# Kernel tuning notes

Hardware: AMD Instinct MI355X
Metric: run time of the kernel (lower is better)

## Reference

```python
import jax, jax.numpy as jnp
import numpy as np

MAX_USERS = 100000
T = 2            # edge_type_count
D = 100          # edge_dim
B = 512
IN_DIM = 200
OUT_DIM = 200
PARTS = [[3, 15], [3, 15, 105, 945]]   # per-schema neighbor partition sizes
RAND_PARTS = [3, 15]
TOTAL_P = sum(PARTS[0]) + sum(PARTS[1])


def _layernorm(x, g, b, eps=1e-6):
    mu = x.mean(axis=-1, keepdims=True)
    var = ((x - mu) ** 2).mean(axis=-1, keepdims=True)
    return (x - mu) / jnp.sqrt(var + eps) * g + b


def _mha(x, Wq, Wk, Wv, Wf, g, b):
    # single-head attention over the second-to-last axis (n_head=1, d_k=d_v=D).
    # NOTE: original only layer-norms q (k, v use the raw input); residual add at end.
    residual = x
    q = _layernorm(x, g, b) @ Wq
    k = x @ Wk
    v = x @ Wv
    attn = jax.nn.softmax(jnp.einsum('...qd,...kd->...qk', q / jnp.sqrt(D), k), axis=-1)
    out = jnp.einsum('...qk,...kd->...qd', attn, v) @ Wf
    return out + residual, attn


def _mean_agg(Ws, Wn, self_x, neigh_x):
    # GraphSAGE-style mean aggregator: relu(concat(self @ Ws, mean(neigh) @ Wn)).
    # neigh_x has shape [N*r, D]; reshape to [N, r, D] and mean over the fanout r.
    n, d = self_x.shape
    neigh_mean = neigh_x.reshape(n, -1, d).mean(axis=1)
    return jax.nn.relu(jnp.concatenate([self_x @ Ws, neigh_mean @ Wn], axis=-1))


def _schema_view(idx, parts, Wself, Wneigh, type_embed, nodeids, neigh_s):
    # neigh_s: [B, T, sum(parts)] node ids for meta-path idx. Returns [B, T, D].
    # Faithful to type_embed[neigh][:, :, :, :, idx, :][:, t, :, t, :] but gathers
    # only the needed (type t, schema idx) slice instead of the huge dense tensor.
    chunks = jnp.split(neigh_s, np.cumsum(parts)[:-1].tolist(), axis=2)
    specs = []
    for t in range(T):
        feats = [type_embed[nodeids, t, idx]]                    # [B, D]
        for c in chunks:
            feats.append(type_embed[c[:, t, :], t, idx].reshape(-1, D))
        for l in range(len(parts)):
            feats = [_mean_agg(Wself[l], Wneigh[l], feats[k], feats[k + 1])
                     for k in range(len(feats) - 1)]
        specs.append(feats[0])
    return jnp.stack(specs, axis=1)


def setup_inputs() -> dict:
    ks = jax.random.split(jax.random.key(0), 32)
    unif = lambda i, s: jax.random.uniform(ks[i], s, dtype=jnp.float32, minval=-1.0, maxval=1.0)
    nrm = lambda i, s, sc=0.1: jax.random.normal(ks[i], s, dtype=jnp.float32) * sc
    inp = {}
    inp['nodeids'] = jax.random.randint(ks[0], (B,), 0, MAX_USERS)
    inp['edgetype'] = jnp.stack([jnp.arange(B), jax.random.randint(ks[1], (B,), 0, T)])
    inp['neighbors'] = jax.random.randint(ks[2], (B, T, TOTAL_P), 0, MAX_USERS)
    inp['random_neighbors'] = jax.random.randint(ks[3], (B, sum(RAND_PARTS)), 0, MAX_USERS)
    inp['base_embed'] = unif(4, (MAX_USERS, IN_DIM))
    inp['type_embed'] = unif(5, (MAX_USERS, T, len(PARTS), D))
    inp['rw_embed'] = unif(6, (MAX_USERS, D))
    inp['reflect'] = nrm(7, (T, D, OUT_DIM), 1.0 / float(np.sqrt(IN_DIM)))
    inp['agg0_self'] = nrm(8, (2, D, D // 2)); inp['agg0_neigh'] = nrm(9, (2, D, D // 2))
    inp['agg1_self'] = nrm(10, (4, D, D // 2)); inp['agg1_neigh'] = nrm(11, (4, D, D // 2))
    inp['rand_self'] = nrm(12, (2, D, D // 2)); inp['rand_neigh'] = nrm(13, (2, D, D // 2))
    inp['vWq'] = nrm(14, (D, D)); inp['vWk'] = nrm(15, (D, D)); inp['vWv'] = nrm(16, (D, D)); inp['vWf'] = nrm(17, (D, D))
    inp['vg'] = jnp.ones((D,), jnp.float32); inp['vb'] = jnp.zeros((D,), jnp.float32)
    inp['mWq'] = nrm(18, (D, D)); inp['mWk'] = nrm(19, (D, D)); inp['mWv'] = nrm(20, (D, D)); inp['mWf'] = nrm(21, (D, D))
    inp['mg'] = jnp.ones((D,), jnp.float32); inp['mb'] = jnp.zeros((D,), jnp.float32)
    return inp


def reference(nodeids, edgetype, neighbors, random_neighbors, base_embed, type_embed,
              rw_embed, reflect, agg0_self, agg0_neigh, agg1_self, agg1_neigh,
              rand_self, rand_neigh, vWq, vWk, vWv, vWf, vg, vb,
              mWq, mWk, mWv, mWf, mg, mb):
    # per-metapath views [B, T, D]
    spec0 = _schema_view(0, PARTS[0], agg0_self, agg0_neigh, type_embed, nodeids,
                         neighbors[:, :, :sum(PARTS[0])])
    spec1 = _schema_view(1, PARTS[1], agg1_self, agg1_neigh, type_embed, nodeids,
                         neighbors[:, :, sum(PARTS[0]):])
    # random-walk view [B, D]
    feats = [rw_embed[nodeids]]
    for c in jnp.split(random_neighbors, np.cumsum(RAND_PARTS)[:-1].tolist(), axis=1):
        feats.append(rw_embed[c].reshape(-1, D))
    for l in range(len(RAND_PARTS)):
        feats = [_mean_agg(rand_self[l], rand_neigh[l], feats[k], feats[k + 1])
                 for k in range(len(feats) - 1)]
    rview = feats[0]
    mv = jnp.stack([spec0, spec1], axis=1)                                   # [B, 2, T, D]
    mv = jnp.concatenate([mv, jnp.broadcast_to(rview[:, None, None, :], (B, 1, T, D))], axis=1)  # [B, 3, T, D]
    mv, _ = _mha(mv, vWq, vWk, vWv, vWf, vg, vb)                             # view attn over type axis T
    mt, _ = _mha(jnp.swapaxes(mv, 1, 2), mWq, mWk, mWv, mWf, mg, mb)         # meta attn over view axis
    pooled = jnp.swapaxes(mt, 1, 2).mean(axis=1)                             # [B, T, D]
    sel = pooled[edgetype[0], edgetype[1]]                                   # [B, D]
    out = jnp.einsum('bd,bdo->bo', sel, reflect[edgetype[1]])                # [B, OUT_DIM]
    res = base_embed[nodeids] + out
    return res / jnp.maximum(jnp.linalg.norm(res, axis=1, keepdims=True), 1e-12)
```

## Files before the change

### kernel.cpp

```cpp
#include <hip/hip_runtime.h>
#include <math.h>


#define NBATCH 512
#define TOTALP 1086
#define RPB 32
#define XSTR 204
#define WSTR 112

struct Seg {
  const float* emb;
  const float* selfp;
  const float* neighp;
  const int*   ids_s;
  const int*   ids_n;
  const float* Ws;
  const float* Wn;
  float*       outp;
  int ss, so;
  int ns, no;
  int estride;
  int ostride;
  int c;
  int r;
  int blk_begin;
};

struct KArgs { Seg seg[14]; int n; };

__global__ __launch_bounds__(256) void agg_kernel(KArgs P) {
  __shared__ float Wsh[100 * WSTR];
  __shared__ float xsh[RPB * XSTR];
  __shared__ int   ids_s_sh[RPB];
  __shared__ int   ids_n_sh[RPB * 9];

  const int blk = blockIdx.x, tid = threadIdx.x;
  int si = 0;
  for (int i = 1; i < P.n; ++i)
    if (blk >= P.seg[i].blk_begin) si = i;
  const Seg sg = P.seg[si];
  const int j0 = (blk - sg.blk_begin) * RPB;
  const int c = sg.c, r = sg.r;

  for (int u = tid; u < 5000; u += 256) {
    int e = u / 50, cc = u - e * 50;
    Wsh[e * WSTR + cc]      = sg.Ws[u];
    Wsh[e * WSTR + 56 + cc] = sg.Wn[u];
  }
  for (int u = tid; u < 1200; u += 256) {
    int e = u / 12, p = u - e * 12;
    Wsh[e * WSTR + (p < 6 ? 50 + p : 100 + p)] = 0.f;
  }
  if (sg.emb) {
    if (tid < RPB) {
      int j = j0 + tid, b = j / c, pos = j - b * c;
      ids_s_sh[tid] = sg.ids_s[(long)b * sg.ss + sg.so + pos];
    }
    for (int u = tid; u < RPB * r; u += 256) {
      int row = u / r, q = u - row * r;
      int j = j0 + row, b = j / c, pos = j - b * c;
      ids_n_sh[u] = sg.ids_n[(long)b * sg.ns + sg.no + pos * r + q];
    }
  }
  __syncthreads();

  const float rinv = 1.f / (float)r;
  for (int u = tid; u < RPB * 25; u += 256) {
    int row = u / 25, q4 = (u - row * 25) * 4;
    float sx, sy, sz, sw, mx = 0.f, my = 0.f, mz = 0.f, mw = 0.f;
    if (sg.emb) {
      const float4 s4 = *(const float4*)(sg.emb + (long)ids_s_sh[row] * sg.estride + q4);
      sx = s4.x; sy = s4.y; sz = s4.z; sw = s4.w;
      for (int rr = 0; rr < r; ++rr) {
        const float4 t = *(const float4*)(sg.emb + (long)ids_n_sh[row * r + rr] * sg.estride + q4);
        mx += t.x; my += t.y; mz += t.z; mw += t.w;
      }
    } else {
      long j = j0 + row;
      const float4 s4 = *(const float4*)(sg.selfp + j * 100 + q4);
      sx = s4.x; sy = s4.y; sz = s4.z; sw = s4.w;
      for (int rr = 0; rr < r; ++rr) {
        const float4 t = *(const float4*)(sg.neighp + (j * r + rr) * 100 + q4);
        mx += t.x; my += t.y; mz += t.z; mw += t.w;
      }
    }
    float4 sv; sv.x = sx; sv.y = sy; sv.z = sz; sv.w = sw;
    float4 mv; mv.x = mx * rinv; mv.y = my * rinv; mv.z = mz * rinv; mv.w = mw * rinv;
    *(float4*)&xsh[row * XSTR + q4]       = sv;
    *(float4*)&xsh[row * XSTR + 100 + q4] = mv;
  }
  __syncthreads();

  if (tid < 224) {
    const int rg = tid / 28, cq = tid - rg * 28;
    const int wcol = 4 * cq;
    const int xoff = (cq < 14) ? 0 : 100;
    float acc[4][4];
#pragma unroll
    for (int i = 0; i < 4; ++i) { acc[i][0] = acc[i][1] = acc[i][2] = acc[i][3] = 0.f; }
    const float* xb = &xsh[(rg * 4) * XSTR + xoff];
#pragma unroll 4
    for (int e = 0; e < 100; ++e) {
      const float4 wv = *(const float4*)&Wsh[e * WSTR + wcol];
#pragma unroll
      for (int i = 0; i < 4; ++i) {
        const float a = xb[i * XSTR + e];
        acc[i][0] = fmaf(a, wv.x, acc[i][0]);
        acc[i][1] = fmaf(a, wv.y, acc[i][1]);
        acc[i][2] = fmaf(a, wv.z, acc[i][2]);
        acc[i][3] = fmaf(a, wv.w, acc[i][3]);
      }
    }
    const int cl = (cq < 14) ? cq : cq - 14;
    if (cl < 13) {
      const int cbase = (cq < 14 ? 0 : 50) + 4 * cl;
      for (int i = 0; i < 4; ++i) {
        const long j = j0 + rg * 4 + i;
        float* op = sg.outp + j * (long)sg.ostride + cbase;
        if (cl < 12) {
          float4 o;
          o.x = fmaxf(acc[i][0], 0.f); o.y = fmaxf(acc[i][1], 0.f);
          o.z = fmaxf(acc[i][2], 0.f); o.w = fmaxf(acc[i][3], 0.f);
          *(float4*)op = o;
        } else {
          op[0] = fmaxf(acc[i][0], 0.f);
          op[1] = fmaxf(acc[i][1], 0.f);
        }
      }
    }
  }
}

__device__ __forceinline__ void attn_step(
    float* xs, int base, int rs, int n,
    const float* Wq, const float* Wk, const float* Wv, const float* Wf,
    const float* g, const float* bb,
    float* ln, float* qq, float* kk, float* vv, float* ot,
    float* sc, float* musd, float* wsh, int tid)
{
  if (tid < n) {
    float mu = 0.f;
    for (int d = 0; d < 100; ++d) mu += xs[base + tid * rs + d];
    mu *= 0.01f;
    float var = 0.f;
    for (int d = 0; d < 100; ++d) {
      float t = xs[base + tid * rs + d] - mu; var = fmaf(t, t, var);
    }
    var *= 0.01f;
    musd[tid * 2]     = mu;
    musd[tid * 2 + 1] = rsqrtf(var + 1e-6f);
  }
  __syncthreads();
  for (int o = tid; o < n * 100; o += 128) {
    int i = o / 100, d = o - i * 100;
    ln[o] = (xs[base + i * rs + d] - musd[i * 2]) * musd[i * 2 + 1] * g[d] + bb[d];
  }
  __syncthreads();

  const bool act = tid < n * 25;
  const int  i   = tid / 25;
  const int  d4  = 4 * (tid - i * 25);
  float aq[4] = {0,0,0,0}, ak[4] = {0,0,0,0}, av[4] = {0,0,0,0};
  for (int ch = 0; ch < 2; ++ch) {
    for (int u = tid; u < 1250; u += 128) {
      int el = u / 25, dd = 4 * (u - el * 25);
      *(float4*)&wsh[el * 300 + dd]       = *(const float4*)&Wq[(ch * 50 + el) * 100 + dd];
      *(float4*)&wsh[el * 300 + 100 + dd] = *(const float4*)&Wk[(ch * 50 + el) * 100 + dd];
      *(float4*)&wsh[el * 300 + 200 + dd] = *(const float4*)&Wv[(ch * 50 + el) * 100 + dd];
    }
    __syncthreads();
    if (act) {
      for (int el = 0; el < 50; ++el) {
        const float lnv = ln[i * 100 + ch * 50 + el];
        const float xv  = xs[base + i * rs + ch * 50 + el];
        const float4 wq = *(const float4*)&wsh[el * 300 + d4];
        const float4 wk = *(const float4*)&wsh[el * 300 + 100 + d4];
        const float4 wv = *(const float4*)&wsh[el * 300 + 200 + d4];
        aq[0] = fmaf(lnv, wq.x, aq[0]); aq[1] = fmaf(lnv, wq.y, aq[1]);
        aq[2] = fmaf(lnv, wq.z, aq[2]); aq[3] = fmaf(lnv, wq.w, aq[3]);
        ak[0] = fmaf(xv,  wk.x, ak[0]); ak[1] = fmaf(xv,  wk.y, ak[1]);
        ak[2] = fmaf(xv,  wk.z, ak[2]); ak[3] = fmaf(xv,  wk.w, ak[3]);
        av[0] = fmaf(xv,  wv.x, av[0]); av[1] = fmaf(xv,  wv.y, av[1]);
        av[2] = fmaf(xv,  wv.z, av[2]); av[3] = fmaf(xv,  wv.w, av[3]);
      }
    }
    __syncthreads();
  }
  if (act) {
#pragma unroll
    for (int jj = 0; jj < 4; ++jj) {
      qq[i * 100 + d4 + jj] = aq[jj];
      kk[i * 100 + d4 + jj] = ak[jj];
      vv[i * 100 + d4 + jj] = av[jj];
    }
  }
  __syncthreads();

  if (tid < n * n) {
    int qi = tid / n, u = tid - qi * n;
    float s = 0.f;
    for (int d = 0; d < 100; ++d) s = fmaf(qq[qi * 100 + d], kk[u * 100 + d], s);
    sc[tid] = s * 0.1f;
  }
  __syncthreads();
  if (tid < n) {
    float mx = sc[tid * n];
    for (int u = 1; u < n; ++u) mx = fmaxf(mx, sc[tid * n + u]);
    float sm = 0.f;
    for (int u = 0; u < n; ++u) {
      float e = expf(sc[tid * n + u] - mx); sc[tid * n + u] = e; sm += e;
    }
    float inv = 1.f / sm;
    for (int u = 0; u < n; ++u) sc[tid * n + u] *= inv;
  }
  __syncthreads();
  for (int o = tid; o < n * 100; o += 128) {
    int ii = o / 100, d = o - ii * 100;
    float a = 0.f;
    for (int u = 0; u < n; ++u) a = fmaf(sc[ii * n + u], vv[u * 100 + d], a);
    ot[o] = a;
  }
  __syncthreads();

  float af[4] = {0,0,0,0};
  for (int ch = 0; ch < 2; ++ch) {
    for (int u = tid; u < 1250; u += 128) {
      int el = u / 25, dd = 4 * (u - el * 25);
      *(float4*)&wsh[el * 100 + dd] = *(const float4*)&Wf[(ch * 50 + el) * 100 + dd];
    }
    __syncthreads();
    if (act) {
      for (int el = 0; el < 50; ++el) {
        const float ov = ot[i * 100 + ch * 50 + el];
        const float4 wf = *(const float4*)&wsh[el * 100 + d4];
        af[0] = fmaf(ov, wf.x, af[0]); af[1] = fmaf(ov, wf.y, af[1]);
        af[2] = fmaf(ov, wf.z, af[2]); af[3] = fmaf(ov, wf.w, af[3]);
      }
    }
    __syncthreads();
  }
  if (act) {
#pragma unroll
    for (int jj = 0; jj < 4; ++jj)
      xs[base + i * rs + d4 + jj] += af[jj];
  }
  __syncthreads();
}

__global__ __launch_bounds__(128) void attn_final_kernel(
    const float* __restrict__ spec, const float* __restrict__ rview,
    const int* __restrict__ nodeids, const int* __restrict__ edgetype,
    const float* __restrict__ base_embed, const float* __restrict__ reflect,
    const float* vWq, const float* vWk, const float* vWv, const float* vWf,
    const float* vg, const float* vb,
    const float* mWq, const float* mWk, const float* mWv, const float* mWf,
    const float* mg, const float* mb,
    float* __restrict__ out)
{
  __shared__ float xs[600], ln[300], qq[300], kk[300], vv[300], ot[300];
  __shared__ float sc[9], musd[6], r200[200], pooled[200], nrmv[1];
  __shared__ float wsh[15000];
  const int b = blockIdx.x, tid = threadIdx.x;

  for (int o = tid; o < 600; o += 128) {
    int v = o / 200, rem = o - v * 200;
    xs[o] = (v < 2) ? spec[(long)b * 400 + o] : rview[(long)b * 100 + (rem % 100)];
  }
  __syncthreads();

  for (int v = 0; v < 3; ++v)
    attn_step(xs, v * 200, 100, 2, vWq, vWk, vWv, vWf, vg, vb,
              ln, qq, kk, vv, ot, sc, musd, wsh, tid);
  for (int t = 0; t < 2; ++t)
    attn_step(xs, t * 100, 200, 3, mWq, mWk, mWv, mWf, mg, mb,
              ln, qq, kk, vv, ot, sc, musd, wsh, tid);

  for (int o = tid; o < 200; o += 128)
    pooled[o] = (xs[o] + xs[200 + o] + xs[400 + o]) * (1.f / 3.f);
  __syncthreads();

  const int  et  = edgetype[NBATCH + b];
  const long nid = nodeids[b];

  float ar[4] = {0,0,0,0};
  if (tid < 50) {
    const float4 be = *(const float4*)&base_embed[nid * 200 + 4 * tid];
    ar[0] = be.x; ar[1] = be.y; ar[2] = be.z; ar[3] = be.w;
  }
  for (int ch = 0; ch < 2; ++ch) {
    for (int u = tid; u < 2500; u += 128) {
      int dl = u / 50, oo = 4 * (u - dl * 50);
      *(float4*)&wsh[dl * 200 + oo] =
          *(const float4*)&reflect[((long)et * 100 + ch * 50 + dl) * 200 + oo];
    }
    __syncthreads();
    if (tid < 50) {
      for (int dl = 0; dl < 50; ++dl) {
        const float pv = pooled[et * 100 + ch * 50 + dl];
        const float4 rv = *(const float4*)&wsh[dl * 200 + 4 * tid];
        ar[0] = fmaf(pv, rv.x, ar[0]); ar[1] = fmaf(pv, rv.y, ar[1]);
        ar[2] = fmaf(pv, rv.z, ar[2]); ar[3] = fmaf(pv, rv.w, ar[3]);
      }
    }
    __syncthreads();
  }
  if (tid < 50) {
    r200[4 * tid]     = ar[0]; r200[4 * tid + 1] = ar[1];
    r200[4 * tid + 2] = ar[2]; r200[4 * tid + 3] = ar[3];
  }
  __syncthreads();
  if (tid == 0) {
    float ss = 0.f;
    for (int o = 0; o < 200; ++o) ss = fmaf(r200[o], r200[o], ss);
    nrmv[0] = 1.f / fmaxf(sqrtf(ss), 1e-12f);
  }
  __syncthreads();
  for (int o = tid; o < 200; o += 128)
    out[(long)b * 200 + o] = r200[o] * nrmv[0];
}

extern "C" void kernel_launch(void* const* d_in, const int* in_sizes, int n_in,
                              void* d_out, int out_size, void* d_ws, size_t ws_size,
                              hipStream_t stream) {
  (void)in_sizes; (void)n_in; (void)out_size; (void)ws_size;
  const int*   nodeids          = (const int*)d_in[0];
  const int*   edgetype         = (const int*)d_in[1];
  const int*   neighbors        = (const int*)d_in[2];
  const int*   random_neighbors = (const int*)d_in[3];
  const float* base_embed       = (const float*)d_in[4];
  const float* type_embed       = (const float*)d_in[5];
  const float* rw_embed         = (const float*)d_in[6];
  const float* reflect          = (const float*)d_in[7];
  const float* agg0_self        = (const float*)d_in[8];
  const float* agg0_neigh       = (const float*)d_in[9];
  const float* agg1_self        = (const float*)d_in[10];
  const float* agg1_neigh       = (const float*)d_in[11];
  const float* rand_self        = (const float*)d_in[12];
  const float* rand_neigh       = (const float*)d_in[13];
  const float* vWq = (const float*)d_in[14];
  const float* vWk = (const float*)d_in[15];
  const float* vWv = (const float*)d_in[16];
  const float* vWf = (const float*)d_in[17];
  const float* vg  = (const float*)d_in[18];
  const float* vb  = (const float*)d_in[19];
  const float* mWq = (const float*)d_in[20];
  const float* mWk = (const float*)d_in[21];
  const float* mWv = (const float*)d_in[22];
  const float* mWf = (const float*)d_in[23];
  const float* mg  = (const float*)d_in[24];
  const float* mb  = (const float*)d_in[25];

  float* ws = (float*)d_ws;
  const long S1r = 147L * NBATCH;
  auto rp = [&](long rows) { return ws + rows * 100; };
  float* spec_f  = ws + 306L * NBATCH * 100;
  float* rview_f = spec_f + (long)NBATCH * 400;

  const int  OFF1[4] = {18, 21, 36, 141};
  const int  FAN1[4] = {3, 5, 7, 9};
  const int  C1[4]   = {1, 3, 15, 105};
  const long CUM1[4]  = {0, 1, 4, 19};
  const long CUM1b[3] = {0, 1, 4};

  KArgs A; long acc = 0;
  auto addg = [&](const float* emb, int estride,
                  const int* isrc, int ss, int so, int c,
                  const int* insrc, int nstr, int no, int r,
                  const float* Ws, const float* Wn, float* outp, int ostride) {
    Seg& s = A.seg[A.n++];
    s.emb = emb; s.selfp = nullptr; s.neighp = nullptr;
    s.ids_s = isrc; s.ids_n = insrc;
    s.Ws = Ws; s.Wn = Wn; s.outp = outp;
    s.ss = ss; s.so = so; s.ns = nstr; s.no = no;
    s.estride = estride; s.ostride = ostride;
    s.c = c; s.r = r; s.blk_begin = (int)acc;
    acc += (long)c * NBATCH / RPB;
  };
  auto addd = [&](const float* selfp, const float* neighp, int c, int r,
                  const float* Ws, const float* Wn, float* outp, int ostride) {
    Seg& s = A.seg[A.n++];
    s.emb = nullptr; s.selfp = selfp; s.neighp = neighp;
    s.ids_s = nullptr; s.ids_n = nullptr;
    s.Ws = Ws; s.Wn = Wn; s.outp = outp;
    s.ss = 0; s.so = 0; s.ns = 0; s.no = 0; s.estride = 0; s.ostride = ostride;
    s.c = c; s.r = r; s.blk_begin = (int)acc;
    acc += (long)c * NBATCH / RPB;
  };

  A.n = 0; acc = 0;
  for (int t = 0; t < 2; ++t)
    for (int k = 0; k < 4; ++k) {
      const float* emb = type_embed + (t * 2 + 1) * 100;
      if (k == 0)
        addg(emb, 400, nodeids, 1, 0, 1,
             neighbors, 2 * TOTALP, t * TOTALP + OFF1[k], FAN1[k],
             agg1_self, agg1_neigh, rp(t * S1r + CUM1[k] * NBATCH), 100);
      else
        addg(emb, 400, neighbors, 2 * TOTALP, t * TOTALP + OFF1[k - 1], C1[k],
             neighbors, 2 * TOTALP, t * TOTALP + OFF1[k], FAN1[k],
             agg1_self, agg1_neigh, rp(t * S1r + CUM1[k] * NBATCH), 100);
    }
  for (int t = 0; t < 2; ++t)
    for (int k = 0; k < 2; ++k) {
      const float* emb = type_embed + (t * 2 + 0) * 100;
      long obase = 294L * NBATCH + (long)t * 4 * NBATCH + (k == 0 ? 0 : 1) * NBATCH;
      if (k == 0)
        addg(emb, 400, nodeids, 1, 0, 1,
             neighbors, 2 * TOTALP, t * TOTALP + 0, 3,
             agg0_self, agg0_neigh, rp(obase), 100);
      else
        addg(emb, 400, neighbors, 2 * TOTALP, t * TOTALP + 0, 3,
             neighbors, 2 * TOTALP, t * TOTALP + 3, 5,
             agg0_self, agg0_neigh, rp(obase), 100);
    }
  for (int k = 0; k < 2; ++k) {
    long obase = 302L * NBATCH + (k == 0 ? 0 : 1) * NBATCH;
    if (k == 0)
      addg(rw_embed, 100, nodeids, 1, 0, 1,
           random_neighbors, 18, 0, 3, rand_self, rand_neigh, rp(obase), 100);
    else
      addg(rw_embed, 100, random_neighbors, 18, 0, 3,
           random_neighbors, 18, 3, 5, rand_self, rand_neigh, rp(obase), 100);
  }
  agg_kernel<<<dim3((unsigned)acc), dim3(256), 0, stream>>>(A);

  A.n = 0; acc = 0;
  for (int t = 0; t < 2; ++t)
    for (int k = 0; k < 3; ++k)
      addd(rp(t * S1r + CUM1[k] * NBATCH), rp(t * S1r + CUM1[k + 1] * NBATCH),
           C1[k], FAN1[k], agg1_self + 5000, agg1_neigh + 5000,
           rp(t * S1r + 124L * NBATCH + CUM1b[k] * NBATCH), 100);
  for (int t = 0; t < 2; ++t)
    addd(rp(294L * NBATCH + (long)t * 4 * NBATCH),
         rp(294L * NBATCH + (long)t * 4 * NBATCH + NBATCH),
         1, 3, agg0_self + 5000, agg0_neigh + 5000, spec_f + t * 100, 400);
  addd(rp(302L * NBATCH), rp(303L * NBATCH), 1, 3,
       rand_self + 5000, rand_neigh + 5000, rview_f, 100);
  agg_kernel<<<dim3((unsigned)acc), dim3(256), 0, stream>>>(A);

  A.n = 0; acc = 0;
  for (int t = 0; t < 2; ++t)
    for (int k = 0; k < 2; ++k)
      addd(rp(t * S1r + 124L * NBATCH + CUM1b[k] * NBATCH),
           rp(t * S1r + 124L * NBATCH + CUM1b[k + 1] * NBATCH),
           C1[k], FAN1[k], agg1_self + 10000, agg1_neigh + 10000,
           rp(t * S1r + 143L * NBATCH + (k == 0 ? 0 : 1) * NBATCH), 100);
  agg_kernel<<<dim3((unsigned)acc), dim3(256), 0, stream>>>(A);

  A.n = 0; acc = 0;
  for (int t = 0; t < 2; ++t)
    addd(rp(t * S1r + 143L * NBATCH), rp(t * S1r + 144L * NBATCH),
         1, 3, agg1_self + 15000, agg1_neigh + 15000,
         spec_f + 200 + t * 100, 400);
  agg_kernel<<<dim3((unsigned)acc), dim3(256), 0, stream>>>(A);

  attn_final_kernel<<<dim3(NBATCH), dim3(128), 0, stream>>>(
      spec_f, rview_f, nodeids, edgetype, base_embed, reflect,
      vWq, vWk, vWv, vWf, vg, vb, mWq, mWk, mWv, mWf, mg, mb,
      (float*)d_out);
}
```

Measured before the change: 657.5 us.

## Compute only the selected edge-type path and read weights directly from global memory

The attention kernel now carries only the query row for the selected edge type through view attention, and only the selected type slice through meta attention. Rows that never reach the output are skipped. It moves to 256 threads with wave-shuffle reductions and drops the large shared-memory weight staging in favour of direct global (L2-cached) weight reads. The aggregation kernel likewise drops its shared-memory weight staging and the padding writes, reading Ws/Wn straight from global memory, which lowers LDS use and may raise occupancy. The trade-off is more global/L2 traffic for weight reads.

New measurement: 707.6 us. 7.6% more time.

```diff
diff --git a/kernel.cpp b/kernel.cpp
--- a/kernel.cpp
+++ b/kernel.cpp
@@ -6,7 +6,6 @@
 #define TOTALP 1086
 #define RPB 32
 #define XSTR 204
-#define WSTR 112
 
 struct Seg {
   const float* emb;
@@ -29,7 +28,6 @@
 struct KArgs { Seg seg[14]; int n; };
 
 __global__ __launch_bounds__(256) void agg_kernel(KArgs P) {
-  __shared__ float Wsh[100 * WSTR];
   __shared__ float xsh[RPB * XSTR];
   __shared__ int   ids_s_sh[RPB];
   __shared__ int   ids_n_sh[RPB * 9];
@@ -42,15 +40,6 @@
   const int j0 = (blk - sg.blk_begin) * RPB;
   const int c = sg.c, r = sg.r;
 
-  for (int u = tid; u < 5000; u += 256) {
-    int e = u / 50, cc = u - e * 50;
-    Wsh[e * WSTR + cc]      = sg.Ws[u];
-    Wsh[e * WSTR + 56 + cc] = sg.Wn[u];
-  }
-  for (int u = tid; u < 1200; u += 256) {
-    int e = u / 12, p = u - e * 12;
-    Wsh[e * WSTR + (p < 6 ? 50 + p : 100 + p)] = 0.f;
-  }
   if (sg.emb) {
     if (tid < RPB) {
       int j = j0 + tid, b = j / c, pos = j - b * c;
@@ -61,8 +50,8 @@
       int j = j0 + row, b = j / c, pos = j - b * c;
       ids_n_sh[u] = sg.ids_n[(long)b * sg.ns + sg.no + pos * r + q];
     }
-  }
-  __syncthreads();
+    __syncthreads();
+  }
 
   const float rinv = 1.f / (float)r;
   for (int u = tid; u < RPB * 25; u += 256) {
@@ -91,232 +80,211 @@
   }
   __syncthreads();
 
-  if (tid < 224) {
-    const int rg = tid / 28, cq = tid - rg * 28;
-    const int wcol = 4 * cq;
-    const int xoff = (cq < 14) ? 0 : 100;
+  if (tid < 208) {
+    const int rg = tid / 26, hq = tid - rg * 26;
+    const int half = hq / 13, q = hq - half * 13;
+    const int col = 4 * q;
+    const float* W = half ? sg.Wn : sg.Ws;
+    const float* xb = &xsh[(rg * 4) * XSTR + half * 100];
     float acc[4][4];
 #pragma unroll
     for (int i = 0; i < 4; ++i) { acc[i][0] = acc[i][1] = acc[i][2] = acc[i][3] = 0.f; }
-    const float* xb = &xsh[(rg * 4) * XSTR + xoff];
-#pragma unroll 4
-    for (int e = 0; e < 100; ++e) {
-      const float4 wv = *(const float4*)&Wsh[e * WSTR + wcol];
+    if (q < 12) {
+#pragma unroll 2
+      for (int e = 0; e < 100; ++e) {
+        const float4 wv = *(const float4*)&W[e * 50 + col];
 #pragma unroll
-      for (int i = 0; i < 4; ++i) {
-        const float a = xb[i * XSTR + e];
-        acc[i][0] = fmaf(a, wv.x, acc[i][0]);
-        acc[i][1] = fmaf(a, wv.y, acc[i][1]);
-        acc[i][2] = fmaf(a, wv.z, acc[i][2]);
-        acc[i][3] = fmaf(a, wv.w, acc[i][3]);
-      }
-    }
-    const int cl = (cq < 14) ? cq : cq - 14;
-    if (cl < 13) {
-      const int cbase = (cq < 14 ? 0 : 50) + 4 * cl;
-      for (int i = 0; i < 4; ++i) {
-        const long j = j0 + rg * 4 + i;
-        float* op = sg.outp + j * (long)sg.ostride + cbase;
-        if (cl < 12) {
-          float4 o;
-          o.x = fmaxf(acc[i][0], 0.f); o.y = fmaxf(acc[i][1], 0.f);
-          o.z = fmaxf(acc[i][2], 0.f); o.w = fmaxf(acc[i][3], 0.f);
-          *(float4*)op = o;
-        } else {
-          op[0] = fmaxf(acc[i][0], 0.f);
-          op[1] = fmaxf(acc[i][1], 0.f);
+        for (int i = 0; i < 4; ++i) {
+          const float a = xb[i * XSTR + e];
+          acc[i][0] = fmaf(a, wv.x, acc[i][0]);
+          acc[i][1] = fmaf(a, wv.y, acc[i][1]);
+          acc[i][2] = fmaf(a, wv.z, acc[i][2]);
+          acc[i][3] = fmaf(a, wv.w, acc[i][3]);
         }
       }
+    } else {
+#pragma unroll 2
+      for (int e = 0; e < 100; ++e) {
+        const float2 wv = *(const float2*)&W[e * 50 + 48];
+#pragma unroll
+        for (int i = 0; i < 4; ++i) {
+          const float a = xb[i * XSTR + e];
+          acc[i][0] = fmaf(a, wv.x, acc[i][0]);
+          acc[i][1] = fmaf(a, wv.y, acc[i][1]);
+        }
+      }
+    }
+    const int ocol = half * 50 + col;
+    for (int i = 0; i < 4; ++i) {
+      const long j = j0 + rg * 4 + i;
+      float* op = sg.outp + j * (long)sg.ostride + ocol;
+      if (q < 12) {
+        float4 o;
+        o.x = fmaxf(acc[i][0], 0.f); o.y = fmaxf(acc[i][1], 0.f);
+        o.z = fmaxf(acc[i][2], 0.f); o.w = fmaxf(acc[i][3], 0.f);
+        *(float4*)op = o;
+      } else {
+        float2 o;
+        o.x = fmaxf(acc[i][0], 0.f); o.y = fmaxf(acc[i][1], 0.f);
+        *(float2*)op = o;
+      }
     }
   }
 }
 
-__device__ __forceinline__ void attn_step(
-    float* xs, int base, int rs, int n,
-    const float* Wq, const float* Wk, const float* Wv, const float* Wf,
-    const float* g, const float* bb,
-    float* ln, float* qq, float* kk, float* vv, float* ot,
-    float* sc, float* musd, float* wsh, int tid)
-{
-  if (tid < n) {
-    float mu = 0.f;
-    for (int d = 0; d < 100; ++d) mu += xs[base + tid * rs + d];
-    mu *= 0.01f;
-    float var = 0.f;
-    for (int d = 0; d < 100; ++d) {
-      float t = xs[base + tid * rs + d] - mu; var = fmaf(t, t, var);
-    }
-    var *= 0.01f;
-    musd[tid * 2]     = mu;
-    musd[tid * 2 + 1] = rsqrtf(var + 1e-6f);
-  }
-  __syncthreads();
-  for (int o = tid; o < n * 100; o += 128) {
-    int i = o / 100, d = o - i * 100;
-    ln[o] = (xs[base + i * rs + d] - musd[i * 2]) * musd[i * 2 + 1] * g[d] + bb[d];
-  }
-  __syncthreads();
-
-  const bool act = tid < n * 25;
-  const int  i   = tid / 25;
-  const int  d4  = 4 * (tid - i * 25);
-  float aq[4] = {0,0,0,0}, ak[4] = {0,0,0,0}, av[4] = {0,0,0,0};
-  for (int ch = 0; ch < 2; ++ch) {
-    for (int u = tid; u < 1250; u += 128) {
-      int el = u / 25, dd = 4 * (u - el * 25);
-      *(float4*)&wsh[el * 300 + dd]       = *(const float4*)&Wq[(ch * 50 + el) * 100 + dd];
-      *(float4*)&wsh[el * 300 + 100 + dd] = *(const float4*)&Wk[(ch * 50 + el) * 100 + dd];
-      *(float4*)&wsh[el * 300 + 200 + dd] = *(const float4*)&Wv[(ch * 50 + el) * 100 + dd];
-    }
-    __syncthreads();
-    if (act) {
-      for (int el = 0; el < 50; ++el) {
-        const float lnv = ln[i * 100 + ch * 50 + el];
-        const float xv  = xs[base + i * rs + ch * 50 + el];
-        const float4 wq = *(const float4*)&wsh[el * 300 + d4];
-        const float4 wk = *(const float4*)&wsh[el * 300 + 100 + d4];
-        const float4 wv = *(const float4*)&wsh[el * 300 + 200 + d4];
-        aq[0] = fmaf(lnv, wq.x, aq[0]); aq[1] = fmaf(lnv, wq.y, aq[1]);
-        aq[2] = fmaf(lnv, wq.z, aq[2]); aq[3] = fmaf(lnv, wq.w, aq[3]);
-        ak[0] = fmaf(xv,  wk.x, ak[0]); ak[1] = fmaf(xv,  wk.y, ak[1]);
-        ak[2] = fmaf(xv,  wk.z, ak[2]); ak[3] = fmaf(xv,  wk.w, ak[3]);
-        av[0] = fmaf(xv,  wv.x, av[0]); av[1] = fmaf(xv,  wv.y, av[1]);
-        av[2] = fmaf(xv,  wv.z, av[2]); av[3] = fmaf(xv,  wv.w, av[3]);
-      }
-    }
-    __syncthreads();
-  }
-  if (act) {
+__device__ __forceinline__ float wave_sum_bcast(float p) {
 #pragma unroll
-    for (int jj = 0; jj < 4; ++jj) {
-      qq[i * 100 + d4 + jj] = aq[jj];
-      kk[i * 100 + d4 + jj] = ak[jj];
-      vv[i * 100 + d4 + jj] = av[jj];
-    }
-  }
-  __syncthreads();
-
-  if (tid < n * n) {
-    int qi = tid / n, u = tid - qi * n;
-    float s = 0.f;
-    for (int d = 0; d < 100; ++d) s = fmaf(qq[qi * 100 + d], kk[u * 100 + d], s);
-    sc[tid] = s * 0.1f;
-  }
-  __syncthreads();
-  if (tid < n) {
-    float mx = sc[tid * n];
-    for (int u = 1; u < n; ++u) mx = fmaxf(mx, sc[tid * n + u]);
-    float sm = 0.f;
-    for (int u = 0; u < n; ++u) {
-      float e = expf(sc[tid * n + u] - mx); sc[tid * n + u] = e; sm += e;
-    }
-    float inv = 1.f / sm;
-    for (int u = 0; u < n; ++u) sc[tid * n + u] *= inv;
-  }
-  __syncthreads();
-  for (int o = tid; o < n * 100; o += 128) {
-    int ii = o / 100, d = o - ii * 100;
-    float a = 0.f;
-    for (int u = 0; u < n; ++u) a = fmaf(sc[ii * n + u], vv[u * 100 + d], a);
-    ot[o] = a;
-  }
-  __syncthreads();
-
-  float af[4] = {0,0,0,0};
-  for (int ch = 0; ch < 2; ++ch) {
-    for (int u = tid; u < 1250; u += 128) {
-      int el = u / 25, dd = 4 * (u - el * 25);
-      *(float4*)&wsh[el * 100 + dd] = *(const float4*)&Wf[(ch * 50 + el) * 100 + dd];
-    }
-    __syncthreads();
-    if (act) {
-      for (int el = 0; el < 50; ++el) {
-        const float ov = ot[i * 100 + ch * 50 + el];
-        const float4 wf = *(const float4*)&wsh[el * 100 + d4];
-        af[0] = fmaf(ov, wf.x, af[0]); af[1] = fmaf(ov, wf.y, af[1]);
-        af[2] = fmaf(ov, wf.z, af[2]); af[3] = fmaf(ov, wf.w, af[3]);
-      }
-    }
-    __syncthreads();
-  }
-  if (act) {
-#pragma unroll
-    for (int jj = 0; jj < 4; ++jj)
-      xs[base + i * rs + d4 + jj] += af[jj];
-  }
-  __syncthreads();
+  for (int off = 32; off; off >>= 1) p += __shfl_down(p, off);
+  return __shfl(p, 0);
 }
 
-__global__ __launch_bounds__(128) void attn_final_kernel(
+__global__ __launch_bounds__(256) void attn_final_kernel(
     const float* __restrict__ spec, const float* __restrict__ rview,
     const int* __restrict__ nodeids, const int* __restrict__ edgetype,
     const float* __restrict__ base_embed, const float* __restrict__ reflect,
-    const float* vWq, const float* vWk, const float* vWv, const float* vWf,
-    const float* vg, const float* vb,
-    const float* mWq, const float* mWk, const float* mWv, const float* mWf,
-    const float* mg, const float* mb,
+    const float* __restrict__ vWq, const float* __restrict__ vWk,
+    const float* __restrict__ vWv, const float* __restrict__ vWf,
+    const float* __restrict__ vg, const float* __restrict__ vb,
+    const float* __restrict__ mWq, const float* __restrict__ mWk,
+    const float* __restrict__ mWv, const float* __restrict__ mWf,
+    const float* __restrict__ mg, const float* __restrict__ mb,
     float* __restrict__ out)
 {
-  __shared__ float xs[600], ln[300], qq[300], kk[300], vv[300], ot[300];
-  __shared__ float sc[9], musd[6], r200[200], pooled[200], nrmv[1];
-  __shared__ float wsh[15000];
+  __shared__ float xs[600], lnb[300], qq[300], kk[300], vv[300], ot[300];
+  __shared__ float sc[9], musd[6], pooled[100], r200[200], nrmv[1];
   const int b = blockIdx.x, tid = threadIdx.x;
-
-  for (int o = tid; o < 600; o += 128) {
+  const int et = edgetype[NBATCH + b];
+  const int nid = nodeids[b];
+
+  for (int o = tid; o < 600; o += 256) {
     int v = o / 200, rem = o - v * 200;
     xs[o] = (v < 2) ? spec[(long)b * 400 + o] : rview[(long)b * 100 + (rem % 100)];
   }
   __syncthreads();
 
-  for (int v = 0; v < 3; ++v)
-    attn_step(xs, v * 200, 100, 2, vWq, vWk, vWv, vWf, vg, vb,
-              ln, qq, kk, vv, ot, sc, musd, wsh, tid);
-  for (int t = 0; t < 2; ++t)
-    attn_step(xs, t * 100, 200, 3, mWq, mWk, mWv, mWf, mg, mb,
-              ln, qq, kk, vv, ot, sc, musd, wsh, tid);
-
-  for (int o = tid; o < 200; o += 128)
-    pooled[o] = (xs[o] + xs[200 + o] + xs[400 + o]) * (1.f / 3.f);
+  for (int v = 0; v < 3; ++v) {
+    float* xq = xs + v * 200 + et * 100;
+    if (tid < 64) {
+      float p = (tid < 50) ? xq[tid] + xq[tid + 50] : 0.f;
+      p = wave_sum_bcast(p);
+      float mu = p * 0.01f, vr = 0.f;
+      if (tid < 50) { float a = xq[tid] - mu, c2 = xq[tid + 50] - mu; vr = a * a + c2 * c2; }
+      vr = wave_sum_bcast(vr);
+      if (tid == 0) { musd[0] = mu; musd[1] = rsqrtf(vr * 0.01f + 1e-6f); }
+    }
+    __syncthreads();
+    if (tid < 100) lnb[tid] = (xq[tid] - musd[0]) * musd[1] * vg[tid] + vb[tid];
+    __syncthreads();
+    for (int o = tid; o < 500; o += 256) {
+      const int m = o / 100, d = o - m * 100;
+      const float* xr; const float* W; float* dst;
+      if (m == 0)      { xr = lnb;                          W = vWq; dst = qq; }
+      else if (m <= 2) { xr = xs + v * 200 + (m - 1) * 100; W = vWk; dst = kk + (m - 1) * 100; }
+      else             { xr = xs + v * 200 + (m - 3) * 100; W = vWv; dst = vv + (m - 3) * 100; }
+      float a = 0.f;
+      for (int e = 0; e < 100; ++e) a = fmaf(xr[e], W[e * 100 + d], a);
+      dst[d] = a;
+    }
+    __syncthreads();
+    if (tid < 2) {
+      float s = 0.f;
+      for (int d = 0; d < 100; ++d) s = fmaf(qq[d], kk[tid * 100 + d], s);
+      sc[tid] = s * 0.1f;
+    }
+    __syncthreads();
+    if (tid == 0) {
+      float mx = fmaxf(sc[0], sc[1]);
+      float e0 = __expf(sc[0] - mx), e1 = __expf(sc[1] - mx);
+      float inv = 1.f / (e0 + e1);
+      sc[0] = e0 * inv; sc[1] = e1 * inv;
+    }
+    __syncthreads();
+    if (tid < 100) ot[tid] = sc[0] * vv[tid] + sc[1] * vv[100 + tid];
+    __syncthreads();
+    if (tid < 100) {
+      float a = 0.f;
+      for (int e = 0; e < 100; ++e) a = fmaf(ot[e], vWf[e * 100 + tid], a);
+      xq[tid] += a;
+    }
+    __syncthreads();
+  }
+
+  {
+    const int w = tid >> 6, l = tid & 63;
+    if (w < 3) {
+      const float* xr = xs + w * 200 + et * 100;
+      float p = (l < 50) ? xr[l] + xr[l + 50] : 0.f;
+      p = wave_sum_bcast(p);
+      float mu = p * 0.01f, vr = 0.f;
+      if (l < 50) { float a = xr[l] - mu, c2 = xr[l + 50] - mu; vr = a * a + c2 * c2; }
+      vr = wave_sum_bcast(vr);
+      if (l == 0) { musd[w * 2] = mu; musd[w * 2 + 1] = rsqrtf(vr * 0.01f + 1e-6f); }
+    }
+    __syncthreads();
+    for (int o = tid; o < 300; o += 256) {
+      int i = o / 100, d = o - i * 100;
+      lnb[o] = (xs[i * 200 + et * 100 + d] - musd[i * 2]) * musd[i * 2 + 1] * mg[d] + mb[d];
+    }
+    __syncthreads();
+    for (int o = tid; o < 900; o += 256) {
+      const int m = o / 300, rr = (o - m * 300) / 100, d = o - m * 300 - rr * 100;
+      const float* xr = (m == 0) ? (lnb + rr * 100) : (xs + rr * 200 + et * 100);
+      const float* W  = (m == 0) ? mWq : (m == 1 ? mWk : mWv);
+      float a = 0.f;
+      for (int e = 0; e < 100; ++e) a = fmaf(xr[e], W[e * 100 + d], a);
+      float* dst = (m == 0) ? qq : (m == 1 ? kk : vv);
+      dst[rr * 100 + d] = a;
+    }
+    __syncthreads();
+    if (tid < 9) {
+      int i = tid / 3, u = tid - i * 3;
+      float s = 0.f;
+      for (int d = 0; d < 100; ++d) s = fmaf(qq[i * 100 + d], kk[u * 100 + d], s);
+      sc[tid] = s * 0.1f;
+    }
+    __syncthreads();
+    if (tid < 3) {
+      float mx = fmaxf(sc[tid * 3], fmaxf(sc[tid * 3 + 1], sc[tid * 3 + 2]));
+      float e0 = __expf(sc[tid * 3] - mx), e1 = __expf(sc[tid * 3 + 1] - mx),
+            e2 = __expf(sc[tid * 3 + 2] - mx);
+      float inv = 1.f / (e0 + e1 + e2);
+      sc[tid * 3] = e0 * inv; sc[tid * 3 + 1] = e1 * inv; sc[tid * 3 + 2] = e2 * inv;
+    }
+    __syncthreads();
+    for (int o = tid; o < 300; o += 256) {
+      int i = o / 100, d = o - i * 100;
+      ot[o] = sc[i * 3] * vv[d] + sc[i * 3 + 1] * vv[100 + d] + sc[i * 3 + 2] * vv[200 + d];
+    }
+    __syncthreads();
+    for (int o = tid; o < 300; o += 256) {
+      int i = o / 100, d = o - i * 100;
+      float a = 0.f;
+      for (int e = 0; e < 100; ++e) a = fmaf(ot[i * 100 + e], mWf[e * 100 + d], a);
+      xs[i * 200 + et * 100 + d] += a;
+    }
+    __syncthreads();
+  }
+
+  if (tid < 100)
+    pooled[tid] = (xs[et * 100 + tid] + xs[200 + et * 100 + tid] +
+                   xs[400 + et * 100 + tid]) * (1.f / 3.f);
   __syncthreads();
-
-  const int  et  = edgetype[NBATCH + b];
-  const long nid = nodeids[b];
-
-  float ar[4] = {0,0,0,0};
-  if (tid < 50) {
-    const float4 be = *(const float4*)&base_embed[nid * 200 + 4 * tid];
-    ar[0] = be.x; ar[1] = be.y; ar[2] = be.z; ar[3] = be.w;
-  }
-  for (int ch = 0; ch < 2; ++ch) {
-    for (int u = tid; u < 2500; u += 128) {
-      int dl = u / 50, oo = 4 * (u - dl * 50);
-      *(float4*)&wsh[dl * 200 + oo] =
-          *(const float4*)&reflect[((long)et * 100 + ch * 50 + dl) * 200 + oo];
-    }
-    __syncthreads();
-    if (tid < 50) {
-      for (int dl = 0; dl < 50; ++dl) {
-        const float pv = pooled[et * 100 + ch * 50 + dl];
-        const float4 rv = *(const float4*)&wsh[dl * 200 + 4 * tid];
-        ar[0] = fmaf(pv, rv.x, ar[0]); ar[1] = fmaf(pv, rv.y, ar[1]);
-        ar[2] = fmaf(pv, rv.z, ar[2]); ar[3] = fmaf(pv, rv.w, ar[3]);
-      }
-    }
-    __syncthreads();
-  }
-  if (tid < 50) {
-    r200[4 * tid]     = ar[0]; r200[4 * tid + 1] = ar[1];
-    r200[4 * tid + 2] = ar[2]; r200[4 * tid + 3] = ar[3];
+  if (tid < 200) {
+    float a = base_embed[(long)nid * 200 + tid];
+    const float* rf = reflect + (long)et * 20000 + tid;
+    for (int d = 0; d < 100; ++d) a = fmaf(pooled[d], rf[d * 200], a);
+    r200[tid] = a;
   }
   __syncthreads();
-  if (tid == 0) {
-    float ss = 0.f;
-    for (int o = 0; o < 200; ++o) ss = fmaf(r200[o], r200[o], ss);
-    nrmv[0] = 1.f / fmaxf(sqrtf(ss), 1e-12f);
+  if (tid < 64) {
+    float p = r200[tid] * r200[tid] + r200[tid + 64] * r200[tid + 64]
+            + r200[tid + 128] * r200[tid + 128];
+    if (tid < 8) p += r200[tid + 192] * r200[tid + 192];
+    p = wave_sum_bcast(p);
+    if (tid == 0) nrmv[0] = 1.f / fmaxf(sqrtf(p), 1e-12f);
   }
   __syncthreads();
-  for (int o = tid; o < 200; o += 128)
-    out[(long)b * 200 + o] = r200[o] * nrmv[0];
+  if (tid < 200) out[(long)b * 200 + tid] = r200[tid] * nrmv[0];
 }
 
 extern "C" void kernel_launch(void* const* d_in, const int* in_sizes, int n_in,
@@ -454,7 +422,7 @@
          spec_f + 200 + t * 100, 400);
   agg_kernel<<<dim3((unsigned)acc), dim3(256), 0, stream>>>(A);
 
-  attn_final_kernel<<<dim3(NBATCH), dim3(128), 0, stream>>>(
+  attn_final_kernel<<<dim3(NBATCH), dim3(256), 0, stream>>>(
       spec_f, rview_f, nodeids, edgetype, base_embed, reflect,
       vWq, vWk, vWv, vWf, vg, vb, mWq, mWk, mWv, mWf, mg, mb,
       (float*)d_out);
```
